# Performance work log

Measured on AMD Instinct MI355X. Metric: run time of the kernel, lower is better.

The kernel has to match this reference:

```python
import jax, jax.numpy as jnp
import numpy as np

N_POINTS = 65536
N0 = 65536
N_NEIGH = 32
K = 15
IN_F = 64
OUT_F = 128
RADIUS = 0.1
KP_EXTENT = 1.2 * RADIUS / 5.0  # config.KP_extent * radius / density_parameter
BN_EPS = 1e-6
NEG_SLOPE = 0.1


def setup_inputs() -> dict:
    key = jax.random.key(0)
    ks = jax.random.split(key, 8)
    cloud_scale = 0.05  # neighbor offsets ~ KP_EXTENT so influences are nonzero
    query_points = jax.random.uniform(ks[0], (N_POINTS, 3), jnp.float32) * cloud_scale
    support_points = jax.random.uniform(ks[1], (N0, 3), jnp.float32) * cloud_scale
    neighbors_indices = jax.random.randint(ks[2], (N_POINTS, N_NEIGH), 0, N0, jnp.int32)
    features = jax.random.normal(ks[3], (N0, IN_F), jnp.float32)
    # fixed kernel point dispositions, scaled to the kernel extent
    kernel_points = jax.random.normal(ks[4], (K, 3), jnp.float32) * (KP_EXTENT / 1.5)
    W = jax.random.normal(ks[5], (K, IN_F, OUT_F), jnp.float32) * np.sqrt(2.0 / OUT_F)
    gamma = jnp.ones((OUT_F,), jnp.float32)
    beta = jnp.zeros((OUT_F,), jnp.float32)
    return {
        "query_points": query_points,
        "support_points": support_points,
        "neighbors_indices": neighbors_indices,
        "features": features,
        "kernel_points": kernel_points,
        "W": W,
        "gamma": gamma,
        "beta": beta,
    }


def reference(query_points, support_points, neighbors_indices, features,
              kernel_points, W, gamma, beta):
    # --- KPConv: gather neighbors, kernel-point linear influence, sum aggregation ---
    # shadow point far away with zero features (handles out-of-range indices in original)
    sp = jnp.concatenate([support_points,
                          jnp.full((1, 3), 1e6, support_points.dtype)], axis=0)
    feat = jnp.concatenate([features,
                            jnp.zeros((1, features.shape[1]), features.dtype)], axis=0)
    neighbors = sp[neighbors_indices]                      # [n, m, 3]
    diffs = neighbors - query_points[:, None, :]           # [n, m, 3]
    # squared distances to each kernel point: [n, m, K]
    sq = jnp.sum((diffs[:, :, None, :] - kernel_points[None, None, :, :]) ** 2, axis=-1)
    # linear influence, 'sum' aggregation mode
    all_w = jnp.maximum(0.0, 1.0 - jnp.sqrt(sq) / KP_EXTENT)  # [n, m, K]
    all_w = jnp.transpose(all_w, (0, 2, 1))                   # [n, K, m]
    neighb_x = feat[neighbors_indices]                        # [n, m, in]
    weighted = jnp.einsum('nkm,nmi->nki', all_w, neighb_x)    # [n, K, in]
    x = jnp.einsum('nki,kio->no', weighted, W)                # [n, out]
    # --- BatchNorm1d (training-mode batch stats) + LeakyReLU(0.1) ---
    mean = jnp.mean(x, axis=0)
    var = jnp.var(x, axis=0)
    x = (x - mean) * jax.lax.rsqrt(var + BN_EPS) * gamma + beta
    return jnp.where(x >= 0, x, NEG_SLOPE * x)
```

## Files before the change

### kernel.cpp

```cpp
#include <hip/hip_runtime.h>

#define NPTS  65536
#define NNEI  32
#define NKP   15
#define INF   64
#define OUTF  128
#define PPB   16
#define KT_N  32
#define NSETS 64
#define INV_KPE 41.666666666666664f
#define BN_EPS 1e-6f
#define NEG_SLOPE 0.1f

typedef __attribute__((ext_vector_type(8))) short  bf16x8;
typedef __attribute__((ext_vector_type(4))) float  f32x4;

__device__ unsigned short g_Wp[KT_N * 8 * 64 * 8];
__device__ unsigned short g_featb[NPTS * INF];
__device__ float g_part[NSETS][2 * OUTF];
__device__ float g_scale[OUTF], g_shift[OUTF];

__device__ __forceinline__ unsigned short f2b(float f) {
    union { float f; unsigned int i; } v; v.f = f;
    unsigned int x = v.i;
    return (unsigned short)((x + 0x7fffu + ((x >> 16) & 1u)) >> 16);
}
__device__ __forceinline__ unsigned int pk2(float a, float b) {
    return (unsigned int)f2b(a) | ((unsigned int)f2b(b) << 16);
}
__device__ __forceinline__ bf16x8 mk8(unsigned int a, unsigned int b,
                                      unsigned int c, unsigned int d) {
    unsigned int t[4] = {a, b, c, d};
    bf16x8 r; __builtin_memcpy(&r, t, 16); return r;
}

__global__ __launch_bounds__(256) void pack_inputs(const float* __restrict__ W,
                                                   const float* __restrict__ feat) {
    const int b = blockIdx.x, t = threadIdx.x;
    if (b < NSETS) g_part[b][t] = 0.0f;
    if (b < 512) {
        int id = b * 256 + t;
        int j  = id & 7;
        int ln = (id >> 3) & 63;
        int nt = (id >> 9) & 7;
        int kt = id >> 12;
        int i  = kt * 32 + ((ln >> 4) * 8) + j;
        int kp = i & 15;
        int ch = i >> 4;
        int o  = nt * 16 + (ln & 15);
        g_Wp[id] = (kp < NKP) ? f2b(W[(kp * 64 + ch) * 128 + o]) : (unsigned short)0;
    } else {
        int id = (b - 512) * 256 + t;
        const float4 v = ((const float4*)feat)[id];
        uint2 r; r.x = pk2(v.x, v.y); r.y = pk2(v.z, v.w);
        ((uint2*)g_featb)[id] = r;
    }
}

__global__ __launch_bounds__(256, 4) void kpconv_fused(
        const float* __restrict__ qp,
        const float* __restrict__ sp,
        const int*   __restrict__ nbr,
        const float* __restrict__ kp,
        float*       __restrict__ out)
{
    __shared__ __align__(16) unsigned short wlds[128 * PPB * 8];
    __shared__ float dbuf[4][128][3];
    __shared__ int   ibuf[4][128];

    const int tid  = threadIdx.x;
    const int lane = tid & 63;
    const int wv   = tid >> 6;
    const int q    = lane >> 4;
    const int c16  = lane & 15;
    const int gp0  = blockIdx.x * PPB + wv * 4;

#pragma unroll
    for (int rep = 0; rep < 2; ++rep) {
        const int pt  = rep * 2 + (lane >> 5);
        const int m   = lane & 31;
        const int gpt = gp0 + pt;
        const int idx = nbr[gpt * NNEI + m];
        ibuf[wv][pt * 32 + m] = idx;
        dbuf[wv][pt * 32 + m][0] = sp[idx * 3 + 0] - qp[gpt * 3 + 0];
        dbuf[wv][pt * 32 + m][1] = sp[idx * 3 + 1] - qp[gpt * 3 + 1];
        dbuf[wv][pt * 32 + m][2] = sp[idx * 3 + 2] - qp[gpt * 3 + 2];
    }
    float kx, ky, kz;
    if (c16 < NKP) { kx = kp[c16 * 3]; ky = kp[c16 * 3 + 1]; kz = kp[c16 * 3 + 2]; }
    else           { kx = ky = kz = 1.0e6f; }

    uint2 dcur[8], dnxt[8];
#pragma unroll
    for (int j = 0; j < 8; ++j) {
        const int idx = ibuf[wv][q * 8 + j];
        dcur[j] = *(const uint2*)&g_featb[idx * INF + c16 * 4];
    }

#pragma unroll
    for (int pt = 0; pt < 4; ++pt) {
        const int pl = wv * 4 + pt;

        if (pt < 3) {
#pragma unroll
            for (int j = 0; j < 8; ++j) {
                const int idx = ibuf[wv][(pt + 1) * 32 + q * 8 + j];
                dnxt[j] = *(const uint2*)&g_featb[idx * INF + c16 * 4];
            }
        }

        float w8[8];
#pragma unroll
        for (int j = 0; j < 8; ++j) {
            const int m = pt * 32 + q * 8 + j;
            const float ex = dbuf[wv][m][0] - kx;
            const float ey = dbuf[wv][m][1] - ky;
            const float ez = dbuf[wv][m][2] - kz;
            const float s  = ex * ex + ey * ey + ez * ez;
            const float w  = 1.0f - __builtin_amdgcn_sqrtf(s) * INV_KPE;
            w8[j] = (w > 0.0f) ? w : 0.0f;
        }
        const bf16x8 af = mk8(pk2(w8[0], w8[1]), pk2(w8[2], w8[3]),
                              pk2(w8[4], w8[5]), pk2(w8[6], w8[7]));

        f32x4 acc[4] = {{0.f,0.f,0.f,0.f},{0.f,0.f,0.f,0.f},
                        {0.f,0.f,0.f,0.f},{0.f,0.f,0.f,0.f}};
#pragma unroll
        for (int nt = 0; nt < 4; ++nt) {
            unsigned int dw[4];
#pragma unroll
            for (int p = 0; p < 4; ++p) {
                const unsigned int lo = (nt < 2) ? dcur[2 * p].x     : dcur[2 * p].y;
                const unsigned int hi = (nt < 2) ? dcur[2 * p + 1].x : dcur[2 * p + 1].y;
                dw[p] = (nt & 1) ? ((lo >> 16) | (hi & 0xffff0000u))
                                 : ((lo & 0xffffu) | (hi << 16));
            }
            acc[nt] = __builtin_amdgcn_mfma_f32_16x16x32_bf16(
                af, mk8(dw[0], dw[1], dw[2], dw[3]), acc[nt], 0, 0, 0);
        }

#pragma unroll
        for (int nt = 0; nt < 4; ++nt) {
            uint2 pv;
            pv.x = pk2(acc[nt][0], acc[nt][1]);
            pv.y = pk2(acc[nt][2], acc[nt][3]);
            const int ibase = (c16 * 4 + nt) * 16 + q * 4;
            const int g   = ibase >> 3;
            const int off = ibase & 7;
            const int plx = pl ^ ((g >> 3) & 7);
            *(uint2*)&wlds[(g * PPB + plx) * 8 + off] = pv;
        }

#pragma unroll
        for (int j = 0; j < 8; ++j) dcur[j] = dnxt[j];
    }
    __syncthreads();

    const int nt0 = wv * 2;
    f32x4 a00 = {0.f,0.f,0.f,0.f}, a01 = {0.f,0.f,0.f,0.f};

    for (int kt = 0; kt < KT_N; ++kt) {
        const int g   = kt * 4 + q;
        const int plx = c16 ^ ((g >> 3) & 7);
        const bf16x8 fa  = *(const bf16x8*)&wlds[(g * PPB + plx) * 8];
        const bf16x8 fb0 = *(const bf16x8*)&g_Wp[((kt * 8 + nt0) * 64 + lane) * 8];
        const bf16x8 fb1 = *(const bf16x8*)&g_Wp[((kt * 8 + nt0 + 1) * 64 + lane) * 8];
        a00 = __builtin_amdgcn_mfma_f32_16x16x32_bf16(fa, fb0, a00, 0, 0, 0);
        a01 = __builtin_amdgcn_mfma_f32_16x16x32_bf16(fa, fb1, a01, 0, 0, 0);
    }

    const int rb = blockIdx.x * PPB + q * 4;
    const int c0 = nt0 * 16 + c16;
    float s0 = 0.f, q0 = 0.f, s1 = 0.f, q1 = 0.f;
#pragma unroll
    for (int r = 0; r < 4; ++r) {
        const float v0 = a00[r], v1 = a01[r];
        out[(rb + r) * OUTF + c0]      = v0;
        out[(rb + r) * OUTF + c0 + 16] = v1;
        s0 += v0; q0 += v0 * v0;
        s1 += v1; q1 += v1 * v1;
    }
    s0 += __shfl_xor(s0, 16); s0 += __shfl_xor(s0, 32);
    q0 += __shfl_xor(q0, 16); q0 += __shfl_xor(q0, 32);
    s1 += __shfl_xor(s1, 16); s1 += __shfl_xor(s1, 32);
    q1 += __shfl_xor(q1, 16); q1 += __shfl_xor(q1, 32);
    const int set = blockIdx.x & (NSETS - 1);
    if (lane < 16) {
        atomicAdd(&g_part[set][nt0 * 16 + lane],            s0);
        atomicAdd(&g_part[set][OUTF + nt0 * 16 + lane],     q0);
        atomicAdd(&g_part[set][nt0 * 16 + 16 + lane],       s1);
        atomicAdd(&g_part[set][OUTF + nt0 * 16 + 16 + lane], q1);
    }
}

__global__ void bn_scaleshift(const float* __restrict__ gamma,
                              const float* __restrict__ beta) {
    const int o = threadIdx.x;
    float s = 0.f, qq = 0.f;
    for (int i = 0; i < NSETS; ++i) { s += g_part[i][o]; qq += g_part[i][OUTF + o]; }
    const float inv_n = 1.0f / (float)NPTS;
    const float mean  = s * inv_n;
    const float var   = qq * inv_n - mean * mean;
    const float sc    = gamma[o] * rsqrtf(var + BN_EPS);
    g_scale[o] = sc;
    g_shift[o] = beta[o] - mean * sc;
}

__global__ __launch_bounds__(256) void bn_norm(float* __restrict__ x) {
    const int id   = blockIdx.x * 256 + threadIdx.x;
    const int base = id * 4;
    const int o0   = base & 127;
    float4 v = *(const float4*)&x[base];
    const float4 sc = *(const float4*)&g_scale[o0];
    const float4 sf = *(const float4*)&g_shift[o0];
    float y0 = v.x * sc.x + sf.x;
    float y1 = v.y * sc.y + sf.y;
    float y2 = v.z * sc.z + sf.z;
    float y3 = v.w * sc.w + sf.w;
    y0 = (y0 >= 0.f) ? y0 : NEG_SLOPE * y0;
    y1 = (y1 >= 0.f) ? y1 : NEG_SLOPE * y1;
    y2 = (y2 >= 0.f) ? y2 : NEG_SLOPE * y2;
    y3 = (y3 >= 0.f) ? y3 : NEG_SLOPE * y3;
    float4 res = {y0, y1, y2, y3};
    *(float4*)&x[base] = res;
}

extern "C" void kernel_launch(void* const* d_in, const int* in_sizes, int n_in,
                              void* d_out, int out_size, void* d_ws, size_t ws_size,
                              hipStream_t stream) {
    const float* qp    = (const float*)d_in[0];
    const float* sp    = (const float*)d_in[1];
    const int*   nbr   = (const int*)d_in[2];
    const float* kp    = (const float*)d_in[4];
    const float* W     = (const float*)d_in[5];
    const float* gamma = (const float*)d_in[6];
    const float* beta  = (const float*)d_in[7];
    const float* feat  = (const float*)d_in[3];
    float* out = (float*)d_out;

    pack_inputs<<<512 + 4096, 256, 0, stream>>>(W, feat);
    kpconv_fused<<<NPTS / PPB, 256, 0, stream>>>(qp, sp, nbr, kp, out);
    bn_scaleshift<<<1, 128, 0, stream>>>(gamma, beta);
    bn_norm<<<(NPTS * OUTF) / (256 * 4), 256, 0, stream>>>(out);
}
```

Baseline: 188.0 us.

## Double points per block and give each wave one output tile over two row tiles

Raises the block to 32 points and 512 threads (8 waves). Each wave now owns a single 16-column output tile and runs two MFMAs over two 16-point row tiles, so each global W fragment load feeds two MFMAs and the W traffic per point halves. The cost is larger LDS per block, 512-thread blocks that can limit occupancy, and two LDS A-fragment reads per k-step.

```diff
diff --git a/kernel.cpp b/kernel.cpp
--- a/kernel.cpp
+++ b/kernel.cpp
@@ -5,7 +5,8 @@
 #define NKP   15
 #define INF   64
 #define OUTF  128
-#define PPB   16
+#define PPB   32
+#define NW    8
 #define KT_N  32
 #define NSETS 64
 #define INV_KPE 41.666666666666664f
@@ -57,7 +58,7 @@
     }
 }
 
-__global__ __launch_bounds__(256, 4) void kpconv_fused(
+__global__ __launch_bounds__(512, 4) void kpconv_fused(
         const float* __restrict__ qp,
         const float* __restrict__ sp,
         const int*   __restrict__ nbr,
@@ -65,8 +66,8 @@
         float*       __restrict__ out)
 {
     __shared__ __align__(16) unsigned short wlds[128 * PPB * 8];
-    __shared__ float dbuf[4][128][3];
-    __shared__ int   ibuf[4][128];
+    __shared__ float dbuf[NW][128][3];
+    __shared__ int   ibuf[NW][128];
 
     const int tid  = threadIdx.x;
     const int lane = tid & 63;
@@ -156,40 +157,37 @@
     }
     __syncthreads();
 
-    const int nt0 = wv * 2;
-    f32x4 a00 = {0.f,0.f,0.f,0.f}, a01 = {0.f,0.f,0.f,0.f};
+    const int nt = wv;
+    f32x4 a0 = {0.f,0.f,0.f,0.f}, a1 = {0.f,0.f,0.f,0.f};
 
     for (int kt = 0; kt < KT_N; ++kt) {
         const int g   = kt * 4 + q;
-        const int plx = c16 ^ ((g >> 3) & 7);
-        const bf16x8 fa  = *(const bf16x8*)&wlds[(g * PPB + plx) * 8];
-        const bf16x8 fb0 = *(const bf16x8*)&g_Wp[((kt * 8 + nt0) * 64 + lane) * 8];
-        const bf16x8 fb1 = *(const bf16x8*)&g_Wp[((kt * 8 + nt0 + 1) * 64 + lane) * 8];
-        a00 = __builtin_amdgcn_mfma_f32_16x16x32_bf16(fa, fb0, a00, 0, 0, 0);
-        a01 = __builtin_amdgcn_mfma_f32_16x16x32_bf16(fa, fb1, a01, 0, 0, 0);
+        const int h   = (g >> 3) & 7;
+        const int plx0 = c16 ^ h;
+        const int plx1 = (c16 + 16) ^ h;
+        const bf16x8 fa0 = *(const bf16x8*)&wlds[(g * PPB + plx0) * 8];
+        const bf16x8 fa1 = *(const bf16x8*)&wlds[(g * PPB + plx1) * 8];
+        const bf16x8 fb  = *(const bf16x8*)&g_Wp[((kt * 8 + nt) * 64 + lane) * 8];
+        a0 = __builtin_amdgcn_mfma_f32_16x16x32_bf16(fa0, fb, a0, 0, 0, 0);
+        a1 = __builtin_amdgcn_mfma_f32_16x16x32_bf16(fa1, fb, a1, 0, 0, 0);
     }
 
     const int rb = blockIdx.x * PPB + q * 4;
-    const int c0 = nt0 * 16 + c16;
-    float s0 = 0.f, q0 = 0.f, s1 = 0.f, q1 = 0.f;
+    const int c0 = nt * 16 + c16;
+    float s = 0.f, qq = 0.f;
 #pragma unroll
     for (int r = 0; r < 4; ++r) {
-        const float v0 = a00[r], v1 = a01[r];
-        out[(rb + r) * OUTF + c0]      = v0;
-        out[(rb + r) * OUTF + c0 + 16] = v1;
-        s0 += v0; q0 += v0 * v0;
-        s1 += v1; q1 += v1 * v1;
-    }
-    s0 += __shfl_xor(s0, 16); s0 += __shfl_xor(s0, 32);
-    q0 += __shfl_xor(q0, 16); q0 += __shfl_xor(q0, 32);
-    s1 += __shfl_xor(s1, 16); s1 += __shfl_xor(s1, 32);
-    q1 += __shfl_xor(q1, 16); q1 += __shfl_xor(q1, 32);
+        const float v0 = a0[r], v1 = a1[r];
+        out[(rb + r) * OUTF + c0]        = v0;
+        out[(rb + 16 + r) * OUTF + c0]   = v1;
+        s += v0 + v1; qq += v0 * v0 + v1 * v1;
+    }
+    s  += __shfl_xor(s, 16);  s  += __shfl_xor(s, 32);
+    qq += __shfl_xor(qq, 16); qq += __shfl_xor(qq, 32);
     const int set = blockIdx.x & (NSETS - 1);
     if (lane < 16) {
-        atomicAdd(&g_part[set][nt0 * 16 + lane],            s0);
-        atomicAdd(&g_part[set][OUTF + nt0 * 16 + lane],     q0);
-        atomicAdd(&g_part[set][nt0 * 16 + 16 + lane],       s1);
-        atomicAdd(&g_part[set][OUTF + nt0 * 16 + 16 + lane], q1);
+        atomicAdd(&g_part[set][nt * 16 + lane],        s);
+        atomicAdd(&g_part[set][OUTF + nt * 16 + lane], qq);
     }
 }
 
@@ -239,7 +237,7 @@
     float* out = (float*)d_out;
 
     pack_inputs<<<512 + 4096, 256, 0, stream>>>(W, feat);
-    kpconv_fused<<<NPTS / PPB, 256, 0, stream>>>(qp, sp, nbr, kp, out);
+    kpconv_fused<<<NPTS / PPB, 512, 0, stream>>>(qp, sp, nbr, kp, out);
     bn_scaleshift<<<1, 128, 0, stream>>>(gamma, beta);
     bn_norm<<<(NPTS * OUTF) / (256 * 4), 256, 0, stream>>>(out);
 }
```

New measurement: 178.5 us. -5.1%, faster.
